# Performance work log

Measured on AMD Instinct MI355X. Metric: run time of the kernel, lower is better.

## Reference

```python
import jax, jax.numpy as jnp
import numpy as np

DIM = 1024
N_HEADS = 16
HEAD_DIM = DIM // N_HEADS  # 64
B, T = 2, 2048


def setup_inputs() -> dict:
    key = jax.random.key(0)
    k1, k2, k3, k4, k5 = jax.random.split(key, 5)
    x = jax.random.normal(k1, (B, T, DIM), dtype=jnp.float32)
    cos = jax.random.uniform(k2, (1, 1, T, HEAD_DIM // 2), dtype=jnp.float32)
    sin = jax.random.uniform(k3, (1, 1, T, HEAD_DIM // 2), dtype=jnp.float32)
    # torch Linear weights: y = x @ W.T ; qkv: [3*dim, dim], out_proj: [dim, dim]
    w_qkv = jax.random.normal(k4, (3 * DIM, DIM), dtype=jnp.float32) * 0.02
    w_out = jax.random.normal(k5, (DIM, DIM), dtype=jnp.float32) * 0.02
    return {"x": x, "cos": cos, "sin": sin, "w_qkv": w_qkv, "w_out": w_out}


def _rope(t, cos, sin):
    # t: [B, H, T, D]; cos/sin broadcast as [1,1,T,D/2]
    t1, t2 = jnp.split(t, 2, axis=-1)
    return jnp.concatenate([t1 * cos - t2 * sin, t1 * sin + t2 * cos], axis=-1)


def reference(x, cos, sin, w_qkv, w_out):
    Bb, Tt, C = x.shape
    qkv = x @ w_qkv.T                                    # [B, T, 3C]
    q, k, v = jnp.split(qkv, 3, axis=-1)
    def heads(t):
        return t.reshape(Bb, Tt, N_HEADS, HEAD_DIM).transpose(0, 2, 1, 3)
    q, k, v = heads(q), heads(k), heads(v)               # [B, H, T, D]
    q = _rope(q, cos, sin)
    k = _rope(k, cos, sin)
    scale = 1.0 / jnp.sqrt(jnp.float32(HEAD_DIM))
    scores = jnp.einsum("bhqd,bhkd->bhqk", q, k) * scale  # [B, H, T, T]
    causal = jnp.tril(jnp.ones((Tt, Tt), dtype=bool))
    scores = jnp.where(causal[None, None], scores, jnp.float32(-jnp.inf))
    attn = jax.nn.softmax(scores, axis=-1)
    out = jnp.einsum("bhqk,bhkd->bhqd", attn, v)          # [B, H, T, D]
    out = out.transpose(0, 2, 1, 3).reshape(Bb, Tt, C)
    return out @ w_out.T
```

## Files before the change

### kernel.cpp

```cpp
#include <hip/hip_runtime.h>

#define DIMC 1024
#define NH   16
#define HD   64
#define BSZ  2
#define TSZ  2048
#define MROWS (BSZ*TSZ)

typedef __attribute__((ext_vector_type(8))) short s16x8;
typedef __attribute__((ext_vector_type(4))) float f32x4;

__device__ __forceinline__ float b2f(unsigned short u) {
  return __uint_as_float(((unsigned)u) << 16);
}
__device__ __forceinline__ unsigned short f2b(float f) {
  unsigned x = __float_as_uint(f);
  unsigned r = x + 0x7fffu + ((x >> 16) & 1u);
  return (unsigned short)(r >> 16);
}
__device__ __forceinline__ unsigned pk2(float a, float b) {
  unsigned r;
  asm("v_cvt_pk_bf16_f32 %0, %1, %2" : "=v"(r) : "v"(a), "v"(b));
  return r;
}
__device__ __forceinline__ float ex2(float x) {
#if __has_builtin(__builtin_amdgcn_exp2f)
  return __builtin_amdgcn_exp2f(x);
#else
  float r; asm("v_exp_f32 %0, %1" : "=v"(r) : "v"(x)); return r;
#endif
}
__device__ __forceinline__ float ldsc(const void* __restrict__ p, int idx, int isf32) {
  return isf32 ? ((const float*)p)[idx] : b2f(((const unsigned short*)p)[idx]);
}

__device__ __forceinline__ void async_cp16(const unsigned short* g, unsigned short* l) {
  __builtin_amdgcn_global_load_lds(
      (const __attribute__((address_space(1))) unsigned int*)g,
      (__attribute__((address_space(3))) unsigned int*)l, 16, 0, 0);
}

__global__ void detect_dtype(const unsigned short* __restrict__ cosp, int* __restrict__ flag) {
  const int i = threadIdx.x;
  const unsigned long long m = __ballot(cosp[i] >= 0x4000u);
  if (i == 0) *flag = (m != 0ull) ? 1 : 0;
}

__global__ __launch_bounds__(256)
void cvt_all(const float* __restrict__ x, const float* __restrict__ wq,
             const float* __restrict__ wo,
             unsigned short* __restrict__ xb, unsigned short* __restrict__ wqb,
             unsigned short* __restrict__ wob, const int* __restrict__ flag) {
  if (*flag == 0) return;
  const unsigned id = blockIdx.x * 256 + threadIdx.x;
  const float* src; unsigned short* dst; unsigned off;
  if (id < 524288u) { src = x; dst = xb; off = id; }
  else if (id < 917504u) { src = wq; dst = wqb; off = id - 524288u; }
  else { src = wo; dst = wob; off = id - 917504u; }
  const float4 a = ((const float4*)src)[off * 2];
  const float4 b = ((const float4*)src)[off * 2 + 1];
  uint4 u;
  u.x = pk2(a.x, a.y); u.y = pk2(a.z, a.w);
  u.z = pk2(b.x, b.y); u.w = pk2(b.z, b.w);
  ((uint4*)dst)[off] = u;
}

__global__ __launch_bounds__(512, 4)
void gemm_qkv128(const void* __restrict__ Aorig, const unsigned short* __restrict__ Aconv,
                 const void* __restrict__ Worig, const unsigned short* __restrict__ Wconv,
                 const void* __restrict__ cosp, const void* __restrict__ sinp,
                 unsigned short* __restrict__ qout,
                 unsigned short* __restrict__ kout,
                 unsigned short* __restrict__ vout,
                 const int* __restrict__ dflag) {
  const int f32flag = *dflag;
  const unsigned short* A = f32flag ? Aconv : (const unsigned short*)Aorig;
  const unsigned short* W = f32flag ? Wconv : (const unsigned short*)Worig;

  const int tid = threadIdx.x;
  const int m0 = blockIdx.y * 128;
  const int n0 = blockIdx.x * 128;

  __shared__ __align__(16) unsigned short s_ab[2 * 16384];

  const int lane = tid & 63;
  const int wave = tid >> 6;
  const int wm = (wave & 3) * 32;
  const int wn = (wave >> 2) * 64;
  const int m16 = lane & 15;
  const int quad = lane >> 4;

  const int srow = lane >> 3;
  const int schunk = (lane & 7) ^ srow;

  const unsigned short* ga = A + (size_t)(m0 + wave * 8 + srow) * DIMC + schunk * 8;
  const unsigned short* gb = W + (size_t)(n0 + wave * 8 + srow) * DIMC + schunk * 8;

  f32x4 acc[2][4];
#pragma unroll
  for (int i = 0; i < 2; ++i)
#pragma unroll
    for (int j = 0; j < 4; ++j) acc[i][j] = (f32x4){0.f, 0.f, 0.f, 0.f};

  auto stage = [&](int b, int kt) {
    unsigned short* sa = s_ab + b * 16384;
#pragma unroll
    for (int u = 0; u < 2; ++u) {
      async_cp16(ga + (size_t)(u * 64) * DIMC + kt, &sa[(u * 64 + wave * 8) * 64]);
      async_cp16(gb + (size_t)(u * 64) * DIMC + kt, &sa[8192 + (u * 64 + wave * 8) * 64]);
    }
  };

  stage(0, 0);
  __syncthreads();

  for (int t = 0; t < 16; ++t) {
    const int cur = t & 1;
    if (t < 15) stage(cur ^ 1, (t + 1) * 64);
    const unsigned short* sa = s_ab + cur * 16384;
    const unsigned short* sb = sa + 8192;
    __builtin_amdgcn_s_setprio(1);
#pragma unroll
    for (int kk = 0; kk < 64; kk += 32) {
      const int cx = ((kk >> 3) + quad) ^ (m16 & 7);
      s16x8 af[2], bf[4];
#pragma unroll
      for (int i = 0; i < 2; ++i)
        af[i] = *(const s16x8*)&sa[(wm + i * 16 + m16) * 64 + cx * 8];
#pragma unroll
      for (int j = 0; j < 4; ++j)
        bf[j] = *(const s16x8*)&sb[(wn + j * 16 + m16) * 64 + cx * 8];
#pragma unroll
      for (int i = 0; i < 2; ++i)
#pragma unroll
        for (int j = 0; j < 4; ++j)
          acc[i][j] = __builtin_amdgcn_mfma_f32_16x16x32_bf16(af[i], bf[j], acc[i][j], 0, 0, 0);
    }
    __builtin_amdgcn_s_setprio(0);
    __syncthreads();
  }

  const int sel = n0 >> 10;
  const int h = ((n0 & 1023) >> 6) + (wave >> 2);
  unsigned short* dst = (sel == 0) ? qout : ((sel == 1) ? kout : vout);
  const float qsc = (sel == 0) ? 0.18033688f : 1.0f;
  unsigned short* tile = s_ab + wave * 2048;
  if (sel < 2) {
#pragma unroll
    for (int i = 0; i < 2; ++i)
#pragma unroll
      for (int r = 0; r < 4; ++r) {
        const int row_l = i * 16 + quad * 4 + r;
        const int t = (m0 + wm + row_l) & 2047;
#pragma unroll
        for (int jg = 0; jg < 2; ++jg) {
          const int d = jg * 16 + m16;
          const float c = ldsc(cosp, t * 32 + d, f32flag);
          const float sn = ldsc(sinp, t * 32 + d, f32flag);
          const float v1 = acc[i][jg][r];
          const float v2 = acc[i][jg + 2][r];
          tile[row_l * 64 + d]      = f2b((v1 * c - v2 * sn) * qsc);
          tile[row_l * 64 + d + 32] = f2b((v1 * sn + v2 * c) * qsc);
        }
      }
  } else {
#pragma unroll
    for (int i = 0; i < 2; ++i)
#pragma unroll
      for (int r = 0; r < 4; ++r) {
        const int row_l = i * 16 + quad * 4 + r;
#pragma unroll
        for (int j = 0; j < 4; ++j)
          tile[row_l * 64 + j * 16 + m16] = f2b(acc[i][j][r]);
      }
  }
#pragma unroll
  for (int s = 0; s < 4; ++s) {
    const int row_l = s * 8 + (lane >> 3);
    const int seg = lane & 7;
    const int mrow_ = m0 + wm + row_l;
    const int bb = mrow_ >> 11;
    const int t = mrow_ & 2047;
    unsigned short* drow = dst + (((size_t)(bb * NH + h)) * TSZ + t) * HD;
    *(uint4*)(drow + seg * 8) = *(const uint4*)&tile[row_l * 64 + seg * 8];
  }
}

__global__ __launch_bounds__(256)
void gemm_out(const void* __restrict__ Aorig, const unsigned short* __restrict__ Aconv,
              const void* __restrict__ Worig, const unsigned short* __restrict__ Wconv,
              void* __restrict__ C, const int* __restrict__ dflag, int Nsz) {
  const int f32flag = *dflag;
  const unsigned short* A = f32flag ? Aconv : (const unsigned short*)Aorig;
  const unsigned short* W = f32flag ? Wconv : (const unsigned short*)Worig;

  const int tid = threadIdx.x;
  const int m0 = blockIdx.y * 128;
  const int n0 = blockIdx.x * 64;

  __shared__ __align__(16) unsigned short s_ab[2 * 12288];

  const int lane = tid & 63;
  const int wave = tid >> 6;
  const int wm = wave * 32;
  const int m16 = lane & 15;
  const int quad = lane >> 4;

  const int srow = lane >> 3;
  const int schunk = (lane & 7) ^ srow;

  const unsigned short* ga = A + (size_t)(m0 + wave * 8 + srow) * DIMC + schunk * 8;
  const unsigned short* gb = W + (size_t)(n0 + wave * 8 + srow) * DIMC + schunk * 8;

  f32x4 acc[2][4];
#pragma unroll
  for (int i = 0; i < 2; ++i)
#pragma unroll
    for (int j = 0; j < 4; ++j) acc[i][j] = (f32x4){0.f, 0.f, 0.f, 0.f};

  auto stage = [&](int b, int kt) {
    unsigned short* sa = s_ab + b * 12288;
#pragma unroll
    for (int u = 0; u < 4; ++u)
      async_cp16(ga + (size_t)(u * 32) * DIMC + kt, &sa[(u * 32 + wave * 8) * 64]);
#pragma unroll
    for (int u = 0; u < 2; ++u)
      async_cp16(gb + (size_t)(u * 32) * DIMC + kt, &sa[8192 + (u * 32 + wave * 8) * 64]);
  };

  stage(0, 0);
  __syncthreads();

  for (int t = 0; t < 16; ++t) {
    const int cur = t & 1;
    if (t < 15) stage(cur ^ 1, (t + 1) * 64);
    const unsigned short* sa = s_ab + cur * 12288;
    const unsigned short* sb = sa + 8192;
    __builtin_amdgcn_s_setprio(1);
#pragma unroll
    for (int kk = 0; kk < 64; kk += 32) {
      const int cx = ((kk >> 3) + quad) ^ (m16 & 7);
      s16x8 af[2], bf[4];
#pragma unroll
      for (int i = 0; i < 2; ++i)
        af[i] = *(const s16x8*)&sa[(wm + i * 16 + m16) * 64 + cx * 8];
#pragma unroll
      for (int j = 0; j < 4; ++j)
        bf[j] = *(const s16x8*)&sb[(j * 16 + m16) * 64 + cx * 8];
#pragma unroll
      for (int i = 0; i < 2; ++i)
#pragma unroll
        for (int j = 0; j < 4; ++j)
          acc[i][j] = __builtin_amdgcn_mfma_f32_16x16x32_bf16(af[i], bf[j], acc[i][j], 0, 0, 0);
    }
    __builtin_amdgcn_s_setprio(0);
    __syncthreads();
  }

  if (f32flag) {
    float* ftile = (float*)s_ab + wave * (32 * 68);
#pragma unroll
    for (int i = 0; i < 2; ++i)
#pragma unroll
      for (int j = 0; j < 4; ++j)
#pragma unroll
        for (int r = 0; r < 4; ++r)
          ftile[(i * 16 + quad * 4 + r) * 68 + j * 16 + m16] = acc[i][j][r];
    float* Cf = (float*)C;
#pragma unroll
    for (int i = 0; i < 2; ++i)
#pragma unroll
      for (int s = 0; s < 4; ++s) {
        const int row_l = i * 16 + s * 4 + (lane >> 4);
        const float4 vv = *(const float4*)&ftile[row_l * 68 + (lane & 15) * 4];
        *(float4*)&Cf[(size_t)(m0 + wm + row_l) * Nsz + n0 + (lane & 15) * 4] = vv;
      }
  } else {
    unsigned short* Ch = (unsigned short*)C;
#pragma unroll
    for (int i = 0; i < 2; ++i)
#pragma unroll
      for (int j = 0; j < 4; ++j)
#pragma unroll
        for (int r = 0; r < 4; ++r) {
          const int mrow_ = m0 + wm + i * 16 + quad * 4 + r;
          const int col = n0 + j * 16 + m16;
          Ch[(size_t)mrow_ * Nsz + col] = f2b(acc[i][j][r]);
        }
  }
}

__device__ __forceinline__ void attn_pass(
    const unsigned short* __restrict__ qgh, const unsigned short* __restrict__ kgh,
    const unsigned short* __restrict__ vgh, unsigned short* __restrict__ outg,
    int b, int h, int qs, int nc, unsigned short* s_k0, unsigned short* s_k1,
    unsigned short* s_v0, unsigned short* s_v1, unsigned short* s_p,
    int tid, int lane, int w, int m16, int quad) {
  const unsigned short* qrow = qgh + (size_t)(qs + m16) * HD;
  const s16x8 bq0 = *(const s16x8*)(qrow + quad * 8);
  const s16x8 bq1 = *(const s16x8*)(qrow + 32 + quad * 8);

  f32x4 oacc[4];
#pragma unroll
  for (int dt = 0; dt < 4; ++dt) oacc[dt] = (f32x4){0.f, 0.f, 0.f, 0.f};
  float m_ = -1e30f, l_ = 0.f;

  const int krow = tid >> 3, kseg = tid & 7;
  const int vkey = tid & 63, vseg = tid >> 6;

  {
    const uint4 pk = *(const uint4*)(kgh + (size_t)krow * HD + kseg * 8);
    const uint4 pv = *(const uint4*)(vgh + (size_t)vkey * HD + vseg * 8);
    *(uint4*)&s_k0[krow * 72 + kseg * 8] = pk;
    const unsigned short* vv = (const unsigned short*)&pv;
#pragma unroll
    for (int jj = 0; jj < 8; ++jj) s_v0[(vseg * 8 + jj) * 72 + vkey] = vv[jj];
  }

  for (int kc = 0; kc < nc; ++kc) {
    unsigned short* sk = (kc & 1) ? s_k1 : s_k0;
    unsigned short* sv = (kc & 1) ? s_v1 : s_v0;
    unsigned short* skN = (kc & 1) ? s_k0 : s_k1;
    unsigned short* svN = (kc & 1) ? s_v0 : s_v1;
    __syncthreads();
    uint4 pk, pv;
    const int pf = (kc + 1 < nc);
    if (pf) {
      pk = *(const uint4*)(kgh + (size_t)((kc + 1) * 64 + krow) * HD + kseg * 8);
      pv = *(const uint4*)(vgh + (size_t)((kc + 1) * 64 + vkey) * HD + vseg * 8);
    }

    if (kc * 64 <= qs + 15) {
      f32x4 sacc[4];
#pragma unroll
      for (int jt = 0; jt < 4; ++jt) sacc[jt] = (f32x4){0.f, 0.f, 0.f, 0.f};
      __builtin_amdgcn_s_setprio(1);
#pragma unroll
      for (int jt = 0; jt < 4; ++jt) {
        const s16x8 ak0 = *(const s16x8*)&sk[(jt * 16 + m16) * 72 + quad * 8];
        sacc[jt] = __builtin_amdgcn_mfma_f32_16x16x32_bf16(ak0, bq0, sacc[jt], 0, 0, 0);
        const s16x8 ak1 = *(const s16x8*)&sk[(jt * 16 + m16) * 72 + 32 + quad * 8];
        sacc[jt] = __builtin_amdgcn_mfma_f32_16x16x32_bf16(ak1, bq1, sacc[jt], 0, 0, 0);
      }
      __builtin_amdgcn_s_setprio(0);

      if (kc * 64 + 63 > qs) {
#pragma unroll
        for (int jt = 0; jt < 4; ++jt)
#pragma unroll
          for (int r = 0; r < 4; ++r)
            if (kc * 64 + jt * 16 + quad * 4 + r > qs + m16) sacc[jt][r] = -1e30f;
      }

      float mx = sacc[0][0];
#pragma unroll
      for (int jt = 0; jt < 4; ++jt)
#pragma unroll
        for (int r = 0; r < 4; ++r) mx = fmaxf(mx, sacc[jt][r]);
      mx = fmaxf(mx, __shfl_xor(mx, 16, 64));
      mx = fmaxf(mx, __shfl_xor(mx, 32, 64));
      if (!__all(mx <= m_ + 8.0f)) {
        const float mn = fmaxf(m_, mx);
        const float alpha = ex2(m_ - mn);
        m_ = mn;
        l_ *= alpha;
#pragma unroll
        for (int dt = 0; dt < 4; ++dt)
#pragma unroll
          for (int r = 0; r < 4; ++r) oacc[dt][r] *= alpha;
      }
      float rs = 0.f;
#pragma unroll
      for (int jt = 0; jt < 4; ++jt)
#pragma unroll
        for (int r = 0; r < 4; ++r) {
          const float p = ex2(sacc[jt][r] - m_);
          sacc[jt][r] = p;
          rs += p;
        }
      rs += __shfl_xor(rs, 16, 64);
      rs += __shfl_xor(rs, 32, 64);
      l_ += rs;

#pragma unroll
      for (int jt = 0; jt < 4; ++jt) {
        uint2 pw;
        pw.x = pk2(sacc[jt][0], sacc[jt][1]);
        pw.y = pk2(sacc[jt][2], sacc[jt][3]);
        *(uint2*)&s_p[(w * 16 + m16) * 72 + jt * 16 + quad * 4] = pw;
      }

      __builtin_amdgcn_s_setprio(1);
#pragma unroll
      for (int kk = 0; kk < 64; kk += 32) {
        const s16x8 bp = *(const s16x8*)&s_p[(w * 16 + m16) * 72 + kk + quad * 8];
#pragma unroll
        for (int dt = 0; dt < 4; ++dt) {
          const s16x8 av = *(const s16x8*)&sv[(dt * 16 + m16) * 72 + kk + quad * 8];
          oacc[dt] = __builtin_amdgcn_mfma_f32_16x16x32_bf16(av, bp, oacc[dt], 0, 0, 0);
        }
      }
      __builtin_amdgcn_s_setprio(0);
    }

    if (pf) {
      *(uint4*)&skN[krow * 72 + kseg * 8] = pk;
      const unsigned short* vv = (const unsigned short*)&pv;
#pragma unroll
      for (int jj = 0; jj < 8; ++jj) svN[(vseg * 8 + jj) * 72 + vkey] = vv[jj];
    }
  }

  const float linv = 1.0f / l_;
#pragma unroll
  for (int dt = 0; dt < 4; ++dt) {
    uint2 ow;
    ow.x = pk2(oacc[dt][0] * linv, oacc[dt][1] * linv);
    ow.y = pk2(oacc[dt][2] * linv, oacc[dt][3] * linv);
    *(uint2*)&s_p[(w * 16 + m16) * 72 + dt * 16 + quad * 4] = ow;
  }
  {
    const int qq = lane >> 2, dseg = lane & 3;
    const uint4 o0 = *(const uint4*)&s_p[(w * 16 + qq) * 72 + dseg * 16];
    const uint4 o1 = *(const uint4*)&s_p[(w * 16 + qq) * 72 + dseg * 16 + 8];
    unsigned short* orow =
        outg + ((size_t)b * TSZ + qs + qq) * DIMC + h * 64 + dseg * 16;
    *(uint4*)orow = o0;
    *(uint4*)(orow + 8) = o1;
  }
}

__global__ __launch_bounds__(512)
void attn_fwd_mfma(const unsigned short* __restrict__ qg,
                   const unsigned short* __restrict__ kg,
                   const unsigned short* __restrict__ vg,
                   unsigned short* __restrict__ outg) {
  const int tid = threadIdx.x;
  const int lane = tid & 63;
  const int w = tid >> 6;
  const int m16 = lane & 15;
  const int quad = lane >> 4;
  const int l = (int)blockIdx.x;
  const int g = (l & 255) >> 5;
  const int p = (l < 256) ? g : (15 - g);
  const int nc = 32 - p;
  const int bh = l & 31;
  const int b = bh >> 4, h = bh & 15;
  const size_t base = (size_t)bh * TSZ * HD;
  const int sub = (w < 4) ? p : (31 - p);
  const int qs = sub * 64 + (w & 3) * 16;

  __shared__ __align__(16) unsigned short s_k0[64 * 72];
  __shared__ __align__(16) unsigned short s_k1[64 * 72];
  __shared__ __align__(16) unsigned short s_v0[64 * 72];
  __shared__ __align__(16) unsigned short s_v1[64 * 72];
  __shared__ __align__(16) unsigned short s_p[128 * 72];

  attn_pass(qg + base, kg + base, vg + base, outg, b, h, qs, nc,
            s_k0, s_k1, s_v0, s_v1, s_p, tid, lane, w, m16, quad);
}

extern "C" void kernel_launch(void* const* d_in, const int* in_sizes, int n_in,
                              void* d_out, int out_size, void* d_ws, size_t ws_size,
                              hipStream_t stream) {
  (void)in_sizes; (void)n_in; (void)out_size; (void)ws_size;
  const void* x    = d_in[0];
  const void* cosp = d_in[1];
  const void* sinp = d_in[2];
  const void* wqkv = d_in[3];
  const void* wout = d_in[4];

  int* dflag = (int*)d_ws;
  const size_t per = (size_t)BSZ * NH * TSZ * HD;
  unsigned short* q = (unsigned short*)((char*)d_ws + 256);
  unsigned short* k = q + per;
  unsigned short* v = k + per;
  unsigned short* attnb = v + per;
  unsigned short* xb   = attnb + (size_t)MROWS * DIMC;
  unsigned short* wqb  = xb + (size_t)MROWS * DIMC;
  unsigned short* wob  = wqb + (size_t)3 * DIMC * DIMC;

  detect_dtype<<<1, 64, 0, stream>>>((const unsigned short*)cosp, dflag);
  cvt_all<<<dim3(4096), dim3(256), 0, stream>>>(
      (const float*)x, (const float*)wqkv, (const float*)wout, xb, wqb, wob, dflag);
  gemm_qkv128<<<dim3(3 * DIMC / 128, MROWS / 128), dim3(512), 0, stream>>>(
      x, xb, wqkv, wqb, cosp, sinp, q, k, v, dflag);
  attn_fwd_mfma<<<dim3(512), dim3(512), 0, stream>>>(q, k, v, attnb);
  gemm_out<<<dim3(DIMC / 64, MROWS / 128), dim3(256), 0, stream>>>(
      attnb, attnb, wout, wob, d_out, dflag, DIMC);
}
```

Measured before the change: 177.7 us.

## Process 128-key chunks per attention iteration with single-buffered K/V

The attention kernel now handles 128 keys per loop iteration instead of 64, so it runs half as many iterations, barriers and online-softmax rescale steps. The double-buffered K/V shared tiles are replaced by a single buffer, with a second barrier before the prefetched data is stored. The K tile row padding changes to 68 elements and the launch bounds now request 4 blocks per SM. The cost is more registers for the wider score tile and a second sync each iteration. The new 136-byte K row stride also breaks 16-byte alignment for the vector LDS accesses.

Result: no change. 174.6 us (-1.8%).

```diff
diff --git a/kernel.cpp b/kernel.cpp
--- a/kernel.cpp
+++ b/kernel.cpp
@@ -290,147 +290,7 @@
   }
 }
 
-__device__ __forceinline__ void attn_pass(
-    const unsigned short* __restrict__ qgh, const unsigned short* __restrict__ kgh,
-    const unsigned short* __restrict__ vgh, unsigned short* __restrict__ outg,
-    int b, int h, int qs, int nc, unsigned short* s_k0, unsigned short* s_k1,
-    unsigned short* s_v0, unsigned short* s_v1, unsigned short* s_p,
-    int tid, int lane, int w, int m16, int quad) {
-  const unsigned short* qrow = qgh + (size_t)(qs + m16) * HD;
-  const s16x8 bq0 = *(const s16x8*)(qrow + quad * 8);
-  const s16x8 bq1 = *(const s16x8*)(qrow + 32 + quad * 8);
-
-  f32x4 oacc[4];
-#pragma unroll
-  for (int dt = 0; dt < 4; ++dt) oacc[dt] = (f32x4){0.f, 0.f, 0.f, 0.f};
-  float m_ = -1e30f, l_ = 0.f;
-
-  const int krow = tid >> 3, kseg = tid & 7;
-  const int vkey = tid & 63, vseg = tid >> 6;
-
-  {
-    const uint4 pk = *(const uint4*)(kgh + (size_t)krow * HD + kseg * 8);
-    const uint4 pv = *(const uint4*)(vgh + (size_t)vkey * HD + vseg * 8);
-    *(uint4*)&s_k0[krow * 72 + kseg * 8] = pk;
-    const unsigned short* vv = (const unsigned short*)&pv;
-#pragma unroll
-    for (int jj = 0; jj < 8; ++jj) s_v0[(vseg * 8 + jj) * 72 + vkey] = vv[jj];
-  }
-
-  for (int kc = 0; kc < nc; ++kc) {
-    unsigned short* sk = (kc & 1) ? s_k1 : s_k0;
-    unsigned short* sv = (kc & 1) ? s_v1 : s_v0;
-    unsigned short* skN = (kc & 1) ? s_k0 : s_k1;
-    unsigned short* svN = (kc & 1) ? s_v0 : s_v1;
-    __syncthreads();
-    uint4 pk, pv;
-    const int pf = (kc + 1 < nc);
-    if (pf) {
-      pk = *(const uint4*)(kgh + (size_t)((kc + 1) * 64 + krow) * HD + kseg * 8);
-      pv = *(const uint4*)(vgh + (size_t)((kc + 1) * 64 + vkey) * HD + vseg * 8);
-    }
-
-    if (kc * 64 <= qs + 15) {
-      f32x4 sacc[4];
-#pragma unroll
-      for (int jt = 0; jt < 4; ++jt) sacc[jt] = (f32x4){0.f, 0.f, 0.f, 0.f};
-      __builtin_amdgcn_s_setprio(1);
-#pragma unroll
-      for (int jt = 0; jt < 4; ++jt) {
-        const s16x8 ak0 = *(const s16x8*)&sk[(jt * 16 + m16) * 72 + quad * 8];
-        sacc[jt] = __builtin_amdgcn_mfma_f32_16x16x32_bf16(ak0, bq0, sacc[jt], 0, 0, 0);
-        const s16x8 ak1 = *(const s16x8*)&sk[(jt * 16 + m16) * 72 + 32 + quad * 8];
-        sacc[jt] = __builtin_amdgcn_mfma_f32_16x16x32_bf16(ak1, bq1, sacc[jt], 0, 0, 0);
-      }
-      __builtin_amdgcn_s_setprio(0);
-
-      if (kc * 64 + 63 > qs) {
-#pragma unroll
-        for (int jt = 0; jt < 4; ++jt)
-#pragma unroll
-          for (int r = 0; r < 4; ++r)
-            if (kc * 64 + jt * 16 + quad * 4 + r > qs + m16) sacc[jt][r] = -1e30f;
-      }
-
-      float mx = sacc[0][0];
-#pragma unroll
-      for (int jt = 0; jt < 4; ++jt)
-#pragma unroll
-        for (int r = 0; r < 4; ++r) mx = fmaxf(mx, sacc[jt][r]);
-      mx = fmaxf(mx, __shfl_xor(mx, 16, 64));
-      mx = fmaxf(mx, __shfl_xor(mx, 32, 64));
-      if (!__all(mx <= m_ + 8.0f)) {
-        const float mn = fmaxf(m_, mx);
-        const float alpha = ex2(m_ - mn);
-        m_ = mn;
-        l_ *= alpha;
-#pragma unroll
-        for (int dt = 0; dt < 4; ++dt)
-#pragma unroll
-          for (int r = 0; r < 4; ++r) oacc[dt][r] *= alpha;
-      }
-      float rs = 0.f;
-#pragma unroll
-      for (int jt = 0; jt < 4; ++jt)
-#pragma unroll
-        for (int r = 0; r < 4; ++r) {
-          const float p = ex2(sacc[jt][r] - m_);
-          sacc[jt][r] = p;
-          rs += p;
-        }
-      rs += __shfl_xor(rs, 16, 64);
-      rs += __shfl_xor(rs, 32, 64);
-      l_ += rs;
-
-#pragma unroll
-      for (int jt = 0; jt < 4; ++jt) {
-        uint2 pw;
-        pw.x = pk2(sacc[jt][0], sacc[jt][1]);
-        pw.y = pk2(sacc[jt][2], sacc[jt][3]);
-        *(uint2*)&s_p[(w * 16 + m16) * 72 + jt * 16 + quad * 4] = pw;
-      }
-
-      __builtin_amdgcn_s_setprio(1);
-#pragma unroll
-      for (int kk = 0; kk < 64; kk += 32) {
-        const s16x8 bp = *(const s16x8*)&s_p[(w * 16 + m16) * 72 + kk + quad * 8];
-#pragma unroll
-        for (int dt = 0; dt < 4; ++dt) {
-          const s16x8 av = *(const s16x8*)&sv[(dt * 16 + m16) * 72 + kk + quad * 8];
-          oacc[dt] = __builtin_amdgcn_mfma_f32_16x16x32_bf16(av, bp, oacc[dt], 0, 0, 0);
-        }
-      }
-      __builtin_amdgcn_s_setprio(0);
-    }
-
-    if (pf) {
-      *(uint4*)&skN[krow * 72 + kseg * 8] = pk;
-      const unsigned short* vv = (const unsigned short*)&pv;
-#pragma unroll
-      for (int jj = 0; jj < 8; ++jj) svN[(vseg * 8 + jj) * 72 + vkey] = vv[jj];
-    }
-  }
-
-  const float linv = 1.0f / l_;
-#pragma unroll
-  for (int dt = 0; dt < 4; ++dt) {
-    uint2 ow;
-    ow.x = pk2(oacc[dt][0] * linv, oacc[dt][1] * linv);
-    ow.y = pk2(oacc[dt][2] * linv, oacc[dt][3] * linv);
-    *(uint2*)&s_p[(w * 16 + m16) * 72 + dt * 16 + quad * 4] = ow;
-  }
-  {
-    const int qq = lane >> 2, dseg = lane & 3;
-    const uint4 o0 = *(const uint4*)&s_p[(w * 16 + qq) * 72 + dseg * 16];
-    const uint4 o1 = *(const uint4*)&s_p[(w * 16 + qq) * 72 + dseg * 16 + 8];
-    unsigned short* orow =
-        outg + ((size_t)b * TSZ + qs + qq) * DIMC + h * 64 + dseg * 16;
-    *(uint4*)orow = o0;
-    *(uint4*)(orow + 8) = o1;
-  }
-}
-
-__global__ __launch_bounds__(512)
+__global__ __launch_bounds__(512, 4)
 void attn_fwd_mfma(const unsigned short* __restrict__ qg,
                    const unsigned short* __restrict__ kg,
                    const unsigned short* __restrict__ vg,
@@ -443,21 +303,165 @@
   const int l = (int)blockIdx.x;
   const int g = (l & 255) >> 5;
   const int p = (l < 256) ? g : (15 - g);
-  const int nc = 32 - p;
+  const int nc = (33 - p) >> 1;
   const int bh = l & 31;
   const int b = bh >> 4, h = bh & 15;
   const size_t base = (size_t)bh * TSZ * HD;
   const int sub = (w < 4) ? p : (31 - p);
   const int qs = sub * 64 + (w & 3) * 16;
 
-  __shared__ __align__(16) unsigned short s_k0[64 * 72];
-  __shared__ __align__(16) unsigned short s_k1[64 * 72];
-  __shared__ __align__(16) unsigned short s_v0[64 * 72];
-  __shared__ __align__(16) unsigned short s_v1[64 * 72];
-  __shared__ __align__(16) unsigned short s_p[128 * 72];
-
-  attn_pass(qg + base, kg + base, vg + base, outg, b, h, qs, nc,
-            s_k0, s_k1, s_v0, s_v1, s_p, tid, lane, w, m16, quad);
+  __shared__ __align__(16) unsigned short s_k[128 * 68];
+  __shared__ __align__(16) unsigned short s_v[64 * 136];
+  __shared__ __align__(16) unsigned short s_p[128 * 136];
+
+  const unsigned short* qgh = qg + base;
+  const unsigned short* kgh = kg + base;
+  const unsigned short* vgh = vg + base;
+
+  const unsigned short* qrow = qgh + (size_t)(qs + m16) * HD;
+  const s16x8 bq0 = *(const s16x8*)(qrow + quad * 8);
+  const s16x8 bq1 = *(const s16x8*)(qrow + 32 + quad * 8);
+
+  f32x4 oacc[4];
+#pragma unroll
+  for (int dt = 0; dt < 4; ++dt) oacc[dt] = (f32x4){0.f, 0.f, 0.f, 0.f};
+  float m_ = -1e30f, l_ = 0.f;
+
+  const int krow = tid >> 3, kseg = tid & 7;
+  const int vkey = tid & 63, vseg = tid >> 6;
+
+  {
+    const uint4 a0 = *(const uint4*)(kgh + (size_t)krow * HD + kseg * 8);
+    const uint4 a1 = *(const uint4*)(kgh + (size_t)(64 + krow) * HD + kseg * 8);
+    const uint4 b0 = *(const uint4*)(vgh + (size_t)vkey * HD + vseg * 8);
+    const uint4 b1 = *(const uint4*)(vgh + (size_t)(64 + vkey) * HD + vseg * 8);
+    *(uint4*)&s_k[krow * 68 + kseg * 8] = a0;
+    *(uint4*)&s_k[(64 + krow) * 68 + kseg * 8] = a1;
+    const unsigned short* v0 = (const unsigned short*)&b0;
+    const unsigned short* v1 = (const unsigned short*)&b1;
+#pragma unroll
+    for (int jj = 0; jj < 8; ++jj) {
+      s_v[(vseg * 8 + jj) * 136 + vkey] = v0[jj];
+      s_v[(vseg * 8 + jj) * 136 + 64 + vkey] = v1[jj];
+    }
+  }
+
+  for (int kc = 0; kc < nc; ++kc) {
+    __syncthreads();
+    uint4 a0, a1, b0, b1;
+    const int pf = (kc + 1 < nc);
+    if (pf) {
+      const size_t ko = (size_t)(kc + 1) * 128;
+      a0 = *(const uint4*)(kgh + (ko + krow) * HD + kseg * 8);
+      a1 = *(const uint4*)(kgh + (ko + 64 + krow) * HD + kseg * 8);
+      b0 = *(const uint4*)(vgh + (ko + vkey) * HD + vseg * 8);
+      b1 = *(const uint4*)(vgh + (ko + 64 + vkey) * HD + vseg * 8);
+    }
+
+    if (kc * 128 <= qs + 15) {
+      f32x4 sacc[8];
+#pragma unroll
+      for (int jt = 0; jt < 8; ++jt) sacc[jt] = (f32x4){0.f, 0.f, 0.f, 0.f};
+      __builtin_amdgcn_s_setprio(1);
+#pragma unroll
+      for (int jt = 0; jt < 8; ++jt) {
+        const s16x8 ak0 = *(const s16x8*)&s_k[(jt * 16 + m16) * 68 + quad * 8];
+        sacc[jt] = __builtin_amdgcn_mfma_f32_16x16x32_bf16(ak0, bq0, sacc[jt], 0, 0, 0);
+        const s16x8 ak1 = *(const s16x8*)&s_k[(jt * 16 + m16) * 68 + 32 + quad * 8];
+        sacc[jt] = __builtin_amdgcn_mfma_f32_16x16x32_bf16(ak1, bq1, sacc[jt], 0, 0, 0);
+      }
+      __builtin_amdgcn_s_setprio(0);
+
+      if (kc * 128 + 127 > qs) {
+#pragma unroll
+        for (int jt = 0; jt < 8; ++jt)
+#pragma unroll
+          for (int r = 0; r < 4; ++r)
+            if (kc * 128 + jt * 16 + quad * 4 + r > qs + m16) sacc[jt][r] = -1e30f;
+      }
+
+      float mx = sacc[0][0];
+#pragma unroll
+      for (int jt = 0; jt < 8; ++jt)
+#pragma unroll
+        for (int r = 0; r < 4; ++r) mx = fmaxf(mx, sacc[jt][r]);
+      mx = fmaxf(mx, __shfl_xor(mx, 16, 64));
+      mx = fmaxf(mx, __shfl_xor(mx, 32, 64));
+      if (!__all(mx <= m_ + 8.0f)) {
+        const float mn = fmaxf(m_, mx);
+        const float alpha = ex2(m_ - mn);
+        m_ = mn;
+        l_ *= alpha;
+#pragma unroll
+        for (int dt = 0; dt < 4; ++dt)
+#pragma unroll
+          for (int r = 0; r < 4; ++r) oacc[dt][r] *= alpha;
+      }
+      float rs = 0.f;
+#pragma unroll
+      for (int jt = 0; jt < 8; ++jt)
+#pragma unroll
+        for (int r = 0; r < 4; ++r) {
+          const float pv_ = ex2(sacc[jt][r] - m_);
+          sacc[jt][r] = pv_;
+          rs += pv_;
+        }
+      rs += __shfl_xor(rs, 16, 64);
+      rs += __shfl_xor(rs, 32, 64);
+      l_ += rs;
+
+#pragma unroll
+      for (int jt = 0; jt < 8; ++jt) {
+        uint2 pw;
+        pw.x = pk2(sacc[jt][0], sacc[jt][1]);
+        pw.y = pk2(sacc[jt][2], sacc[jt][3]);
+        *(uint2*)&s_p[(w * 16 + m16) * 136 + jt * 16 + quad * 4] = pw;
+      }
+
+      __builtin_amdgcn_s_setprio(1);
+#pragma unroll
+      for (int kk = 0; kk < 128; kk += 32) {
+        const s16x8 bp = *(const s16x8*)&s_p[(w * 16 + m16) * 136 + kk + quad * 8];
+#pragma unroll
+        for (int dt = 0; dt < 4; ++dt) {
+          const s16x8 av = *(const s16x8*)&s_v[(dt * 16 + m16) * 136 + kk + quad * 8];
+          oacc[dt] = __builtin_amdgcn_mfma_f32_16x16x32_bf16(av, bp, oacc[dt], 0, 0, 0);
+        }
+      }
+      __builtin_amdgcn_s_setprio(0);
+    }
+
+    __syncthreads();
+    if (pf) {
+      *(uint4*)&s_k[krow * 68 + kseg * 8] = a0;
+      *(uint4*)&s_k[(64 + krow) * 68 + kseg * 8] = a1;
+      const unsigned short* v0 = (const unsigned short*)&b0;
+      const unsigned short* v1 = (const unsigned short*)&b1;
+#pragma unroll
+      for (int jj = 0; jj < 8; ++jj) {
+        s_v[(vseg * 8 + jj) * 136 + vkey] = v0[jj];
+        s_v[(vseg * 8 + jj) * 136 + 64 + vkey] = v1[jj];
+      }
+    }
+  }
+
+  const float linv = 1.0f / l_;
+#pragma unroll
+  for (int dt = 0; dt < 4; ++dt) {
+    uint2 ow;
+    ow.x = pk2(oacc[dt][0] * linv, oacc[dt][1] * linv);
+    ow.y = pk2(oacc[dt][2] * linv, oacc[dt][3] * linv);
+    *(uint2*)&s_p[(w * 16 + m16) * 136 + dt * 16 + quad * 4] = ow;
+  }
+  {
+    const int qq = lane >> 2, dseg = lane & 3;
+    const uint4 o0 = *(const uint4*)&s_p[(w * 16 + qq) * 136 + dseg * 16];
+    const uint4 o1 = *(const uint4*)&s_p[(w * 16 + qq) * 136 + dseg * 16 + 8];
+    unsigned short* orow =
+        outg + ((size_t)b * TSZ + qs + qq) * DIMC + h * 64 + dseg * 16;
+    *(uint4*)orow = o0;
+    *(uint4*)(orow + 8) = o1;
+  }
 }
 
 extern "C" void kernel_launch(void* const* d_in, const int* in_sizes, int n_in,
```
